# Optimization experiments

Measured on AMD Instinct MI355X. Metric: run time of the kernel, lower is better.

The kernel has to match this reference:

```python
import jax, jax.numpy as jnp
import numpy as np

HIDDEN = 128
IN = 2
OUT = 2

def setup_inputs() -> dict:
    key = jax.random.key(0)
    ks = jax.random.split(key, 12)
    B, S = 1024, 512
    s_ih = 1.0 / np.sqrt(HIDDEN)
    return {
        "x0": jax.random.normal(ks[0], (B, OUT), jnp.float32),
        "v_seq": jax.random.normal(ks[1], (B, S, IN), jnp.float32),
        # GRU params (PyTorch layout: gates ordered r, z, n)
        "W_ih": jax.random.uniform(ks[2], (3 * HIDDEN, IN), jnp.float32, -s_ih, s_ih),
        "W_hh": jax.random.uniform(ks[3], (3 * HIDDEN, HIDDEN), jnp.float32, -s_ih, s_ih),
        "b_ih": jax.random.uniform(ks[4], (3 * HIDDEN,), jnp.float32, -s_ih, s_ih),
        "b_hh": jax.random.uniform(ks[5], (3 * HIDDEN,), jnp.float32, -s_ih, s_ih),
        # output Linear hidden -> OUT
        "W_out": jax.random.uniform(ks[6], (OUT, HIDDEN), jnp.float32, -s_ih, s_ih),
        "b_out": jax.random.uniform(ks[7], (OUT,), jnp.float32, -s_ih, s_ih),
        # residual predictor: Linear(OUT+IN -> HIDDEN//2), ReLU, Linear(-> OUT)
        "W_r1": jax.random.uniform(ks[8], (HIDDEN // 2, OUT + IN), jnp.float32, -0.5, 0.5),
        "b_r1": jax.random.uniform(ks[9], (HIDDEN // 2,), jnp.float32, -0.5, 0.5),
        "W_r2": jax.random.uniform(ks[10], (OUT, HIDDEN // 2), jnp.float32, -s_ih, s_ih),
        "b_r2": jax.random.uniform(ks[11], (OUT,), jnp.float32, -s_ih, s_ih),
    }

def _gru_seq(v_seq, W_ih, W_hh, b_ih, b_hh):
    B, S, _ = v_seq.shape
    H = W_hh.shape[1]
    # precompute input projections for all timesteps: [B,S,3H]
    xp = jnp.einsum('bsi,gi->bsg', v_seq, W_ih) + b_ih
    xp = jnp.swapaxes(xp, 0, 1)  # [S,B,3H]

    def step(h, xp_t):
        gh = h @ W_hh.T + b_hh  # [B,3H]
        xr, xz, xn = jnp.split(xp_t, 3, axis=-1)
        hr, hz, hn = jnp.split(gh, 3, axis=-1)
        r = jax.nn.sigmoid(xr + hr)
        z = jax.nn.sigmoid(xz + hz)
        n = jnp.tanh(xn + r * hn)
        h_new = (1.0 - z) * n + z * h
        return h_new, h_new

    h0 = jnp.zeros((B, H), v_seq.dtype)
    _, h_seq = jax.lax.scan(step, h0, xp)
    return jnp.swapaxes(h_seq, 0, 1)  # [B,S,H]

def reference(x0, v_seq, W_ih, W_hh, b_ih, b_hh, W_out, b_out, W_r1, b_r1, W_r2, b_r2):
    h_seq = _gru_seq(v_seq, W_ih, W_hh, b_ih, b_hh)
    x_pred = jnp.einsum('bsh,oh->bso', h_seq, W_out) + b_out  # [B,S,OUT]
    # In the torch loop, x_prev at step t is x0 for t=0 else x_pred[:,t-1],
    # so the loop vectorizes as a shift along time.
    x_prev = jnp.concatenate([x0[:, None, :], x_pred[:, :-1, :]], axis=1)
    # input_size == output_size, so v_t[:, :OUT] == v_t (no padding branch)
    ri = jnp.concatenate([x_prev, v_seq], axis=-1)  # [B,S,OUT+IN]
    hid = jax.nn.relu(jnp.einsum('bsf,hf->bsh', ri, W_r1) + b_r1)
    residual = jnp.einsum('bsh,oh->bso', hid, W_r2) + b_r2
    physics_pred = x_prev + v_seq + residual
    physics_violations = x_pred - physics_pred
    return (x_pred, physics_violations)
```

## Files before the change

### kernel.cpp

```cpp
#include <hip/hip_runtime.h>
#include <stdint.h>

#define BB 1024
#define SS 512
#define HH 128
#define MM 4
#define BLK 512
#define NBLK (BB / MM)
#define HPS 136
#define RS 32
#define RStr 144

typedef float f32x4 __attribute__((ext_vector_type(4)));
typedef float f32x2 __attribute__((ext_vector_type(2)));
typedef _Float16 f16x8 __attribute__((ext_vector_type(8)));

#define LO_SCALE 2048.0f
#define LO_INV   (1.0f / 2048.0f)

__device__ __forceinline__ float sigf(float x) { return 1.0f / (1.0f + __expf(-x)); }
__device__ __forceinline__ float tanh_fast(float x) { return 2.0f / (1.0f + __expf(-2.0f * x)) - 1.0f; }

__global__ __launch_bounds__(BLK, 2) void pig_kernel(
    const float* __restrict__ x0, const float* __restrict__ v_seq,
    const float* __restrict__ W_ih, const float* __restrict__ W_hh,
    const float* __restrict__ b_ih, const float* __restrict__ b_hh,
    const float* __restrict__ W_out, const float* __restrict__ b_out,
    const float* __restrict__ W_r1, const float* __restrict__ b_r1,
    const float* __restrict__ W_r2, const float* __restrict__ b_r2,
    float* __restrict__ out)
{
    __shared__ __align__(16) _Float16 hpack[2][16 * HPS];
    __shared__ __align__(16) _Float16 ring[RS * 4 * RStr];
    __shared__ __align__(16) float    v_lds[SS * 8];
    __shared__ __align__(16) float    xs[RS + 1][8];
    __shared__ __align__(16) float    wpk[64][8];
    __shared__ float xc[2][8];

    const int tid  = threadIdx.x;
    const int wave = tid >> 6;
    const int lane = tid & 63;
    const int quad = lane >> 4;
    const int col  = lane & 15;
    const int row0 = blockIdx.x * MM;
    const int j    = wave * 16 + col;

    f16x8 whi[3][4];
#pragma unroll
    for (int nt = 0; nt < 3; ++nt) {
        const int g = nt * HH + j;
#pragma unroll
        for (int kk = 0; kk < 4; ++kk) {
            const float* p = W_hh + g * HH + kk * 32 + quad * 8;
            f16x8 fh;
#pragma unroll
            for (int i = 0; i < 8; ++i) fh[i] = (_Float16)p[i];
            whi[nt][kk] = fh;
        }
    }

    const float wr0 = W_ih[j*2],        wr1 = W_ih[j*2+1];
    const float wz0 = W_ih[(HH+j)*2],   wz1 = W_ih[(HH+j)*2+1];
    const float wn0 = W_ih[(2*HH+j)*2], wn1 = W_ih[(2*HH+j)*2+1];
    const float br  = b_ih[j]      + b_hh[j];
    const float bz  = b_ih[HH+j]   + b_hh[HH+j];
    const float bni = b_ih[2*HH+j];
    const float bnh = b_hh[2*HH+j];

    const int g8  = tid >> 3;
    const int l8  = tid & 7;
    const int oA  = g8 & 1;
    const int mA  = (g8 >> 1) & 3;
    const int tt8 = g8 >> 3;
    float woA[16];
#pragma unroll
    for (int i = 0; i < 16; ++i) woA[i] = W_out[oA * HH + l8 * 16 + i];
    const float boA = b_out[oA];

    const int qB = tid & 3;
    const int mB = (tid >> 2) & 3;
    const int tB = tid >> 4;
    const float b2B = b_r2[qB & 1];

    for (int idx = tid; idx < 2 * 16 * HPS; idx += BLK) ((_Float16*)hpack)[idx] = (_Float16)0.0f;
    for (int idx = tid; idx < MM * SS * 2; idx += BLK) {
        const int m = idx >> 10, i = idx & 1023;
        v_lds[(i >> 1) * 8 + m * 2 + (i & 1)] = v_seq[(size_t)(row0 + m) * (SS * 2) + i];
    }
    if (tid < 64) {
        wpk[tid][0] = W_r1[tid*4];   wpk[tid][1] = W_r1[tid*4+1];
        wpk[tid][2] = W_r1[tid*4+2]; wpk[tid][3] = W_r1[tid*4+3];
        wpk[tid][4] = b_r1[tid];
        wpk[tid][5] = W_r2[tid];     wpk[tid][6] = W_r2[64 + tid];
        wpk[tid][7] = 0.0f;
    }
    if (tid < 8)
        xc[0][tid] = x0[(size_t)(row0 + (tid >> 1)) * 2 + (tid & 1)];
    __syncthreads();

    float hold = 0.0f;
    for (int t = 0; t < SS; ++t) {
        const int cur = t & 1, nxt = cur ^ 1;

        f32x4 aH0 = {0,0,0,0}, aH1 = {0,0,0,0}, aH2 = {0,0,0,0};
#pragma unroll
        for (int kk = 0; kk < 4; ++kk) {
            f16x8 af = *(const f16x8*)&hpack[cur][col * HPS + kk * 32 + quad * 8];
            aH0 = __builtin_amdgcn_mfma_f32_16x16x32_f16(af, whi[0][kk], aH0, 0, 0, 0);
            aH1 = __builtin_amdgcn_mfma_f32_16x16x32_f16(af, whi[1][kk], aH1, 0, 0, 0);
            aH2 = __builtin_amdgcn_mfma_f32_16x16x32_f16(af, whi[2][kk], aH2, 0, 0, 0);
        }
        const float gh0 = aH0[0] + aH0[1] * LO_INV;
        const float gh1 = aH1[0] + aH1[1] * LO_INV;
        const float gh2 = aH2[0] + aH2[1] * LO_INV;

        const f32x2 vv2 = *(const f32x2*)&v_lds[t * 8 + quad * 2];
        const float r = sigf(gh0 + vv2[0]*wr0 + vv2[1]*wr1 + br);
        const float z = sigf(gh1 + vv2[0]*wz0 + vv2[1]*wz1 + bz);
        const float n = tanh_fast(vv2[0]*wn0 + vv2[1]*wn1 + bni + r * (gh2 + bnh));
        hold = n + z * (hold - n);

        const _Float16 hh = (_Float16)hold;
        hpack[nxt][(4*quad)     * HPS + j] = hh;
        hpack[nxt][(4*quad + 1) * HPS + j] = (_Float16)((hold - (float)hh) * LO_SCALE);
        ring[((t & (RS-1)) * 4 + quad) * RStr + j] = hh;

        __syncthreads();

        if ((t & (RS - 1)) == (RS - 1)) {
            const int f  = t >> 5;
            const int t0 = t - (RS - 1);

            if (tid < 8) xs[0][tid] = xc[f & 1][tid];
#pragma unroll
            for (int p = 0; p < 4; ++p) {
                const int tt = p * 8 + tt8;
                const f16x8 h0 = *(const f16x8*)&ring[(tt * 4 + mA) * RStr + l8 * 16];
                const f16x8 h1 = *(const f16x8*)&ring[(tt * 4 + mA) * RStr + l8 * 16 + 8];
                float acc = 0.0f;
#pragma unroll
                for (int i = 0; i < 8; ++i) {
                    acc += (float)h0[i] * woA[i];
                    acc += (float)h1[i] * woA[8 + i];
                }
                acc += __shfl_xor(acc, 1, 64);
                acc += __shfl_xor(acc, 2, 64);
                acc += __shfl_xor(acc, 4, 64);
                if (l8 == 0) xs[1 + tt][mA * 2 + oA] = acc + boA;
            }
            __syncthreads();

            {
                const float xp0 = xs[tB][mB*2], xp1 = xs[tB][mB*2+1];
                const f32x2 vt2 = *(const f32x2*)&v_lds[(t0 + tB) * 8 + mB * 2];
                float rss0 = 0.0f, rss1 = 0.0f;
#pragma unroll
                for (int uu = 0; uu < 16; ++uu) {
                    const int u = qB * 16 + uu;
                    const f32x4 wA = *(const f32x4*)&wpk[u][0];
                    const f32x4 wB = *(const f32x4*)&wpk[u][4];
                    const float hu = fmaxf(wB[0] + wA[0]*xp0 + wA[1]*xp1 + wA[2]*vt2[0] + wA[3]*vt2[1], 0.0f);
                    rss0 += hu * wB[1];
                    rss1 += hu * wB[2];
                }
                rss0 += __shfl_xor(rss0, 1, 64);
                rss1 += __shfl_xor(rss1, 1, 64);
                rss0 += __shfl_xor(rss0, 2, 64);
                rss1 += __shfl_xor(rss1, 2, 64);
                if (qB < 2) {
                    const int o = qB;
                    const float xpred = xs[tB + 1][mB*2 + o];
                    const float xpv   = xs[tB][mB*2 + o];
                    const float vv    = v_lds[(t0 + tB) * 8 + mB*2 + o];
                    const float resid = (o ? rss1 : rss0) + b2B;
                    const float viol  = xpred - (xpv + vv + resid);
                    const size_t base = (size_t)(row0 + mB) * (SS * 2) + (t0 + tB) * 2 + o;
                    out[base] = xpred;
                    out[(size_t)BB * SS * 2 + base] = viol;
                }
                if (tid < 8) xc[(f + 1) & 1][tid] = xs[RS][tid];
            }
            __syncthreads();
        }
    }
}

extern "C" void kernel_launch(void* const* d_in, const int* in_sizes, int n_in,
                              void* d_out, int out_size, void* d_ws, size_t ws_size,
                              hipStream_t stream) {
    pig_kernel<<<dim3(NBLK), dim3(BLK), 0, stream>>>(
        (const float*)d_in[0],  (const float*)d_in[1],  (const float*)d_in[2],
        (const float*)d_in[3],  (const float*)d_in[4],  (const float*)d_in[5],
        (const float*)d_in[6],  (const float*)d_in[7],  (const float*)d_in[8],
        (const float*)d_in[9],  (const float*)d_in[10], (const float*)d_in[11],
        (float*)d_out);
}
```

Before: 395.0 us.

## Repack hidden-state LDS layout, use hardware exp2/rcp, prefetch next input

Replaces the padded row-major hidden-state buffer with a packed 1024-element layout whose read and write indices are chosen so each lane's MFMA A-fragment load is contiguous, which should reduce LDS bank conflicts on the serial recurrence path. Gate nonlinearities now use the amdgcn exp2 and rcp builtins with folded log2e constants, plus fmaf fusions. The next timestep's v values are loaded before the barrier to hide LDS latency. The ring stride also shrinks from 144 to 136. The approximate rcp/exp2 may change numerics slightly.

Measured after the change: 343.6 us. -13.0%, faster.

```diff
diff --git a/kernel.cpp b/kernel.cpp
--- a/kernel.cpp
+++ b/kernel.cpp
@@ -7,9 +7,8 @@
 #define MM 4
 #define BLK 512
 #define NBLK (BB / MM)
-#define HPS 136
 #define RS 32
-#define RStr 144
+#define RStr 136
 
 typedef float f32x4 __attribute__((ext_vector_type(4)));
 typedef float f32x2 __attribute__((ext_vector_type(2)));
@@ -17,9 +16,10 @@
 
 #define LO_SCALE 2048.0f
 #define LO_INV   (1.0f / 2048.0f)
-
-__device__ __forceinline__ float sigf(float x) { return 1.0f / (1.0f + __expf(-x)); }
-__device__ __forceinline__ float tanh_fast(float x) { return 2.0f / (1.0f + __expf(-2.0f * x)) - 1.0f; }
+#define L2E      1.44269504088896f
+
+__device__ __forceinline__ float rcp_fast(float x)  { return __builtin_amdgcn_rcpf(x); }
+__device__ __forceinline__ float exp2_fast(float x) { return __builtin_amdgcn_exp2f(x); }
 
 __global__ __launch_bounds__(BLK, 2) void pig_kernel(
     const float* __restrict__ x0, const float* __restrict__ v_seq,
@@ -30,7 +30,7 @@
     const float* __restrict__ W_r2, const float* __restrict__ b_r2,
     float* __restrict__ out)
 {
-    __shared__ __align__(16) _Float16 hpack[2][16 * HPS];
+    __shared__ __align__(16) _Float16 hp2[2][1024];
     __shared__ __align__(16) _Float16 ring[RS * 4 * RStr];
     __shared__ __align__(16) float    v_lds[SS * 8];
     __shared__ __align__(16) float    xs[RS + 1][8];
@@ -67,6 +67,10 @@
     const float bni = b_ih[2*HH+j];
     const float bnh = b_hh[2*HH+j];
 
+    const int rr    = ((col >> 2) << 1) | (col & 1);
+    const int rbase = quad * 64 + rr * 8;
+    const int wbase = ((j >> 5) << 8) + (((j >> 3) & 3) << 6) + (quad << 4) + (j & 7);
+
     const int g8  = tid >> 3;
     const int l8  = tid & 7;
     const int oA  = g8 & 1;
@@ -82,7 +86,7 @@
     const int tB = tid >> 4;
     const float b2B = b_r2[qB & 1];
 
-    for (int idx = tid; idx < 2 * 16 * HPS; idx += BLK) ((_Float16*)hpack)[idx] = (_Float16)0.0f;
+    for (int idx = tid; idx < 2 * 1024; idx += BLK) ((_Float16*)hp2)[idx] = (_Float16)0.0f;
     for (int idx = tid; idx < MM * SS * 2; idx += BLK) {
         const int m = idx >> 10, i = idx & 1023;
         v_lds[(i >> 1) * 8 + m * 2 + (i & 1)] = v_seq[(size_t)(row0 + m) * (SS * 2) + i];
@@ -99,31 +103,38 @@
     __syncthreads();
 
     float hold = 0.0f;
+    f32x2 vv2 = *(const f32x2*)&v_lds[quad * 2];
+
     for (int t = 0; t < SS; ++t) {
         const int cur = t & 1, nxt = cur ^ 1;
 
         f32x4 aH0 = {0,0,0,0}, aH1 = {0,0,0,0}, aH2 = {0,0,0,0};
+        const _Float16* hb = &hp2[cur][rbase];
 #pragma unroll
         for (int kk = 0; kk < 4; ++kk) {
-            f16x8 af = *(const f16x8*)&hpack[cur][col * HPS + kk * 32 + quad * 8];
+            f16x8 af = *(const f16x8*)&hb[kk * 256];
             aH0 = __builtin_amdgcn_mfma_f32_16x16x32_f16(af, whi[0][kk], aH0, 0, 0, 0);
             aH1 = __builtin_amdgcn_mfma_f32_16x16x32_f16(af, whi[1][kk], aH1, 0, 0, 0);
             aH2 = __builtin_amdgcn_mfma_f32_16x16x32_f16(af, whi[2][kk], aH2, 0, 0, 0);
         }
-        const float gh0 = aH0[0] + aH0[1] * LO_INV;
-        const float gh1 = aH1[0] + aH1[1] * LO_INV;
-        const float gh2 = aH2[0] + aH2[1] * LO_INV;
-
-        const f32x2 vv2 = *(const f32x2*)&v_lds[t * 8 + quad * 2];
-        const float r = sigf(gh0 + vv2[0]*wr0 + vv2[1]*wr1 + br);
-        const float z = sigf(gh1 + vv2[0]*wz0 + vv2[1]*wz1 + bz);
-        const float n = tanh_fast(vv2[0]*wn0 + vv2[1]*wn1 + bni + r * (gh2 + bnh));
-        hold = n + z * (hold - n);
+        const float gh0 = fmaf(aH0[1], LO_INV, aH0[0]);
+        const float gh1 = fmaf(aH1[1], LO_INV, aH1[0]);
+        const float gh2 = fmaf(aH2[1], LO_INV, aH2[0]);
+
+        const float ra = gh0 + vv2[0]*wr0 + vv2[1]*wr1 + br;
+        const float r  = rcp_fast(1.0f + exp2_fast(ra * (-L2E)));
+        const float za = gh1 + vv2[0]*wz0 + vv2[1]*wz1 + bz;
+        const float z  = rcp_fast(1.0f + exp2_fast(za * (-L2E)));
+        const float na = vv2[0]*wn0 + vv2[1]*wn1 + bni + r * (gh2 + bnh);
+        const float n  = fmaf(2.0f, rcp_fast(1.0f + exp2_fast(na * (-2.0f * L2E))), -1.0f);
+        hold = fmaf(z, hold - n, n);
 
         const _Float16 hh = (_Float16)hold;
-        hpack[nxt][(4*quad)     * HPS + j] = hh;
-        hpack[nxt][(4*quad + 1) * HPS + j] = (_Float16)((hold - (float)hh) * LO_SCALE);
+        hp2[nxt][wbase]     = hh;
+        hp2[nxt][wbase + 8] = (_Float16)((hold - (float)hh) * LO_SCALE);
         ring[((t & (RS-1)) * 4 + quad) * RStr + j] = hh;
+
+        vv2 = *(const f32x2*)&v_lds[((t + 1) & (SS - 1)) * 8 + quad * 2];
 
         __syncthreads();
 
```
